# Kernel tuning notes

Hardware: AMD Instinct MI355X
Metric: run time of the kernel (lower is better)

Reference implementation:

```python
import jax, jax.numpy as jnp
import numpy as np

NUM_EXPERTS = 64
TOP_K = 2
AUX_COEF = 0.01
Z_COEF = 0.001
INIT_STD = 0.02


def setup_inputs() -> dict:
    key = jax.random.key(0)
    k1, k2 = jax.random.split(key)
    B, S, D = 4, 4096, 2048
    x = jax.random.normal(k1, (B, S, D), dtype=jnp.float32)
    gate_w = jax.random.normal(k2, (NUM_EXPERTS, D), dtype=jnp.float32) * INIT_STD
    return {"x": x, "gate_w": gate_w}


def reference(x, gate_w):
    B, S, D = x.shape
    E, K = NUM_EXPERTS, TOP_K
    # gate linear: (B,S,D) @ (D,E) -> (B,S,E), cast to fp32 like .float()
    logits = jnp.einsum('bsd,ed->bse', x, gate_w).astype(jnp.float32)
    weights = jax.nn.softmax(logits, axis=-1)
    top_weights, top_indices = jax.lax.top_k(weights, K)
    top_weights = top_weights / jnp.sum(top_weights, axis=-1, keepdims=True)
    # load-balance aux loss (training branch)
    flat_idx = top_indices.reshape(-1)
    tokens_per_expert = jax.ops.segment_sum(
        jnp.ones_like(flat_idx, dtype=jnp.float32), flat_idx, num_segments=E)
    f = tokens_per_expert / (B * S * K)
    P = jnp.mean(weights, axis=(0, 1))
    balance_loss = E * jnp.sum(f * P)
    z_loss = jnp.mean(jnp.square(jax.nn.logsumexp(logits, axis=-1)))
    aux_loss = AUX_COEF * balance_loss + Z_COEF * z_loss
    return top_indices, top_weights, aux_loss
```

## Files before the change

### kernel.cpp

```cpp
#include <hip/hip_runtime.h>
#include <math.h>

#define NTOK 16384
#define DDIM 2048
#define NEXP 64
#define NKQ 8
#define KSLICE 256
#define TPB 128

typedef __attribute__((ext_vector_type(8))) short bf16x8;
typedef __attribute__((ext_vector_type(4))) float f32x4;


__device__ __forceinline__ unsigned short f2bf(float f) {
    unsigned int u = __builtin_bit_cast(unsigned int, f);
    u += 0x7fffu + ((u >> 16) & 1u);
    return (unsigned short)(u >> 16);
}
__device__ __forceinline__ float bf2f(unsigned short s) {
    return __builtin_bit_cast(float, ((unsigned int)s) << 16);
}
__device__ __forceinline__ void split3(float x, unsigned short &h,
                                       unsigned short &m, unsigned short &l) {
    h = f2bf(x);
    float r1 = x - bf2f(h);
    m = f2bf(r1);
    float r2 = r1 - bf2f(m);
    l = f2bf(r2);
}

__global__ void k_wpack(const float* __restrict__ gw, unsigned short* __restrict__ wp) {
    int idx = blockIdx.x * 256 + threadIdx.x;
    int lane = idx & 63;
    int ks   = (idx >> 6) & 63;
    int eg   = idx >> 12;
    int e  = eg * 16 + (lane & 15);
    int k0 = ks * 32 + (lane >> 4) * 8;
    const float* src = gw + (size_t)e * DDIM + k0;
    union { unsigned short s[8]; uint4 v; } H, M, L;
    #pragma unroll
    for (int j = 0; j < 8; ++j) split3(src[j], H.s[j], M.s[j], L.s[j]);
    size_t fb = (size_t)(eg * 64 + ks) * 1536 + lane * 8;
    *(uint4*)(wp + fb)        = H.v;
    *(uint4*)(wp + fb + 512)  = M.v;
    *(uint4*)(wp + fb + 1024) = L.v;
}

__global__ __launch_bounds__(512, 4)
void k_gemm(const float* __restrict__ x, const unsigned short* __restrict__ wp,
            float* __restrict__ part) {
    __shared__ __align__(16) char Ws[49152];

    const int tid  = threadIdx.x;
    const int kq   = blockIdx.x & 7;
    const int tok0 = (blockIdx.x >> 3) * TPB;

    const int lane = tid & 63;
    const int wv   = tid >> 6;
    const int tau  = lane & 15;
    const int kap  = lane >> 4;

    const float* xb = x + (size_t)(tok0 + wv * 16 + tau) * DDIM
                        + kq * KSLICE + kap * 8;
    float4 xf[4][2];
    #pragma unroll
    for (int i = 0; i < 4; ++i) {
        xf[i][0] = *(const float4*)(xb + i * 32);
        xf[i][1] = *(const float4*)(xb + i * 32 + 4);
    }

    f32x4 acc[4];
    #pragma unroll
    for (int eg = 0; eg < 4; ++eg) acc[eg] = (f32x4){0.f, 0.f, 0.f, 0.f};

    for (int h = 0; h < 2; ++h) {
        if (h) __syncthreads();
        {
            const char* wsrc = (const char*)wp + (size_t)(kq * 8 + h * 4) * 3072;
            #pragma unroll
            for (int eg = 0; eg < 4; ++eg) {
                const char* s = wsrc + (size_t)eg * 196608;
                char* d = Ws + eg * 12288;
                #pragma unroll
                for (int r = 0; r < 2; ++r) {
                    int idx = r * 512 + tid;
                    if (idx < 768)
                        *(uint4*)(d + idx * 16) = *(const uint4*)(s + idx * 16);
                }
            }
        }
        __syncthreads();
        #pragma unroll
        for (int ks = 0; ks < 4; ++ks) {
            float4 a = xf[ks][0], b = xf[ks][1];
            union U8 { unsigned short s[8]; bf16x8 v; };
            U8 Ah, Am, Al;
            float in[8] = {a.x, a.y, a.z, a.w, b.x, b.y, b.z, b.w};
            #pragma unroll
            for (int j = 0; j < 8; ++j) split3(in[j], Ah.s[j], Am.s[j], Al.s[j]);

            if (h == 0) {
                xf[ks][0] = *(const float4*)(xb + 128 + ks * 32);
                xf[ks][1] = *(const float4*)(xb + 128 + ks * 32 + 4);
            }

            #pragma unroll
            for (int eg = 0; eg < 4; ++eg) {
                const char* wb = Ws + eg * 12288 + ks * 3072 + lane * 16;
                bf16x8 Bh = *(const bf16x8*)(wb);
                bf16x8 Bm = *(const bf16x8*)(wb + 1024);
                bf16x8 Bl = *(const bf16x8*)(wb + 2048);
                acc[eg] = __builtin_amdgcn_mfma_f32_16x16x32_bf16(Ah.v, Bh, acc[eg], 0, 0, 0);
                acc[eg] = __builtin_amdgcn_mfma_f32_16x16x32_bf16(Ah.v, Bm, acc[eg], 0, 0, 0);
                acc[eg] = __builtin_amdgcn_mfma_f32_16x16x32_bf16(Am.v, Bh, acc[eg], 0, 0, 0);
                acc[eg] = __builtin_amdgcn_mfma_f32_16x16x32_bf16(Ah.v, Bl, acc[eg], 0, 0, 0);
                acc[eg] = __builtin_amdgcn_mfma_f32_16x16x32_bf16(Al.v, Bh, acc[eg], 0, 0, 0);
                acc[eg] = __builtin_amdgcn_mfma_f32_16x16x32_bf16(Am.v, Bm, acc[eg], 0, 0, 0);
            }
        }
    }

    float* pb = part + ((size_t)kq * NTOK + tok0 + wv * 16) * 64;
    #pragma unroll
    for (int eg = 0; eg < 4; ++eg)
        #pragma unroll
        for (int j = 0; j < 4; ++j)
            pb[(kap * 4 + j) * 64 + eg * 16 + tau] = acc[eg][j];
}

__global__ __launch_bounds__(256)
void k_reduce(const float* __restrict__ part, float* __restrict__ out,
              float* __restrict__ gcnt, float* __restrict__ gP,
              float* __restrict__ gz) {
    __shared__ float Ps[NEXP], Cnt[NEXP], Zs;
    const int tid = threadIdx.x;
    if (tid < NEXP) { Ps[tid] = 0.f; Cnt[tid] = 0.f; }
    if (tid == 0) Zs = 0.f;
    __syncthreads();

    const int lane = tid & 63;
    const int wv   = tid >> 6;
    const int t0   = blockIdx.x * 16 + wv * 4;

    float v[4][8];
    #pragma unroll
    for (int i = 0; i < 4; ++i)
        #pragma unroll
        for (int q = 0; q < 8; ++q)
            v[i][q] = part[((size_t)q * NTOK + t0 + i) * 64 + lane];

    float Pacc = 0.f, zacc = 0.f;
    #pragma unroll
    for (int i = 0; i < 4; ++i) {
        float l = ((v[i][0] + v[i][1]) + (v[i][2] + v[i][3]))
                + ((v[i][4] + v[i][5]) + (v[i][6] + v[i][7]));
        float mx = l;
        #pragma unroll
        for (int off = 32; off > 0; off >>= 1) mx = fmaxf(mx, __shfl_xor(mx, off));
        float s = expf(l - mx);
        float sum = s;
        #pragma unroll
        for (int off = 32; off > 0; off >>= 1) sum += __shfl_xor(sum, off);
        Pacc += s / sum;

        unsigned long long b1 = __ballot(l == mx);
        int i1 = __ffsll(b1) - 1;
        float l2 = (lane == i1) ? -INFINITY : l;
        float m2 = l2;
        #pragma unroll
        for (int off = 32; off > 0; off >>= 1) m2 = fmaxf(m2, __shfl_xor(m2, off));
        unsigned long long b2 = __ballot(l2 == m2);
        int i2 = __ffsll(b2) - 1;

        if (lane == 0) {
            float s2  = expf(m2 - mx);
            float inv = 1.f / (1.f + s2);
            int gt = t0 + i;
            ((float2*)out)[gt]              = make_float2((float)i1, (float)i2);
            ((float2*)(out + 2 * NTOK))[gt] = make_float2(inv, s2 * inv);
            atomicAdd(&Cnt[i1], 1.f);
            atomicAdd(&Cnt[i2], 1.f);
            float lse = mx + logf(sum);
            zacc += lse * lse;
        }
    }
    atomicAdd(&Ps[lane], Pacc);
    if (lane == 0) atomicAdd(&Zs, zacc);
    __syncthreads();

    if (tid < NEXP) {
        atomicAdd(&gcnt[tid], Cnt[tid]);
        atomicAdd(&gP[tid],   Ps[tid]);
    }
    if (tid == 0) atomicAdd(gz, Zs);
}

__global__ void k_final(const float* __restrict__ ws, float* __restrict__ out) {
    int lane = threadIdx.x;
    float v = ws[lane] * ws[64 + lane];
    #pragma unroll
    for (int off = 32; off > 0; off >>= 1) v += __shfl_xor(v, off);
    if (lane == 0) {
        float bal = 64.f * v / (32768.f * 16384.f);
        float z   = ws[128] / 16384.f;
        out[4 * NTOK] = 0.01f * bal + 0.001f * z;
    }
}

extern "C" void kernel_launch(void* const* d_in, const int* in_sizes, int n_in,
                              void* d_out, int out_size, void* d_ws, size_t ws_size,
                              hipStream_t stream) {
    const float* x  = (const float*)d_in[0];
    const float* gw = (const float*)d_in[1];
    float* out = (float*)d_out;
    float* wsf = (float*)d_ws;
    unsigned short* wp = (unsigned short*)((char*)d_ws + 1024);
    float* part = (float*)((char*)d_ws + (1 << 20));

    hipMemsetAsync(d_ws, 0, 516, stream);
    k_wpack<<<64, 256, 0, stream>>>(gw, wp);
    k_gemm<<<NKQ * (NTOK / TPB), 512, 0, stream>>>(x, wp, part);
    k_reduce<<<NTOK / 16, 256, 0, stream>>>(part, out, wsf, wsf + 64, wsf + 128);
    k_final<<<1, 64, 0, stream>>>(wsf, out);
}
```

Measured before the change: 86.64 us.

## Use packed bf16 convert for splits and prefetch weight tiles via registers

Replaces the scalar software float-to-bf16 rounding in the 3-way split with the hardware v_cvt_pk_bf16_f32 instruction, which converts two floats at once. Re-lays out the packed weight buffer so that each k-quarter's tiles are contiguous. The GEMM now loads all weight tiles for both halves through registers, fetching the second half while the first half computes. This hides global load latency behind the MFMA work and cuts ALU cost in the split, at the price of 24 extra VGPRs for the weight prefetch.

```diff
diff --git a/kernel.cpp b/kernel.cpp
--- a/kernel.cpp
+++ b/kernel.cpp
@@ -12,21 +12,15 @@
 typedef __attribute__((ext_vector_type(4))) float f32x4;
 
 
-__device__ __forceinline__ unsigned short f2bf(float f) {
-    unsigned int u = __builtin_bit_cast(unsigned int, f);
-    u += 0x7fffu + ((u >> 16) & 1u);
-    return (unsigned short)(u >> 16);
-}
-__device__ __forceinline__ float bf2f(unsigned short s) {
-    return __builtin_bit_cast(float, ((unsigned int)s) << 16);
-}
-__device__ __forceinline__ void split3(float x, unsigned short &h,
-                                       unsigned short &m, unsigned short &l) {
-    h = f2bf(x);
-    float r1 = x - bf2f(h);
-    m = f2bf(r1);
-    float r2 = r1 - bf2f(m);
-    l = f2bf(r2);
+__device__ __forceinline__ void split3pk(float a, float b,
+                                         unsigned &H, unsigned &M, unsigned &L) {
+    asm("v_cvt_pk_bf16_f32 %0, %1, %2" : "=v"(H) : "v"(a), "v"(b));
+    float ra = a - __builtin_bit_cast(float, H << 16);
+    float rb = b - __builtin_bit_cast(float, H & 0xffff0000u);
+    asm("v_cvt_pk_bf16_f32 %0, %1, %2" : "=v"(M) : "v"(ra), "v"(rb));
+    float sa = ra - __builtin_bit_cast(float, M << 16);
+    float sb = rb - __builtin_bit_cast(float, M & 0xffff0000u);
+    asm("v_cvt_pk_bf16_f32 %0, %1, %2" : "=v"(L) : "v"(sa), "v"(sb));
 }
 
 __global__ void k_wpack(const float* __restrict__ gw, unsigned short* __restrict__ wp) {
@@ -37,13 +31,15 @@
     int e  = eg * 16 + (lane & 15);
     int k0 = ks * 32 + (lane >> 4) * 8;
     const float* src = gw + (size_t)e * DDIM + k0;
-    union { unsigned short s[8]; uint4 v; } H, M, L;
-    #pragma unroll
-    for (int j = 0; j < 8; ++j) split3(src[j], H.s[j], M.s[j], L.s[j]);
-    size_t fb = (size_t)(eg * 64 + ks) * 1536 + lane * 8;
-    *(uint4*)(wp + fb)        = H.v;
-    *(uint4*)(wp + fb + 512)  = M.v;
-    *(uint4*)(wp + fb + 1024) = L.v;
+    uint4 H, M, L;
+    split3pk(src[0], src[1], H.x, M.x, L.x);
+    split3pk(src[2], src[3], H.y, M.y, L.y);
+    split3pk(src[4], src[5], H.z, M.z, L.z);
+    split3pk(src[6], src[7], H.w, M.w, L.w);
+    size_t fb = ((size_t)ks * 12 + eg * 3) * 512 + lane * 8;
+    *(uint4*)(wp + fb)        = H;
+    *(uint4*)(wp + fb + 512)  = M;
+    *(uint4*)(wp + fb + 1024) = L;
 }
 
 __global__ __launch_bounds__(512, 4)
@@ -54,7 +50,6 @@
     const int tid  = threadIdx.x;
     const int kq   = blockIdx.x & 7;
     const int tok0 = (blockIdx.x >> 3) * TPB;
-
     const int lane = tid & 63;
     const int wv   = tid >> 6;
     const int tau  = lane & 15;
@@ -69,35 +64,39 @@
         xf[i][1] = *(const float4*)(xb + i * 32 + 4);
     }
 
+    const char* wsrc = (const char*)wp + (size_t)(kq * 8) * 12288;
+    uint4 wreg[6];
+    #pragma unroll
+    for (int r = 0; r < 6; ++r)
+        wreg[r] = *(const uint4*)(wsrc + (r * 512 + tid) * 16);
+
     f32x4 acc[4];
     #pragma unroll
     for (int eg = 0; eg < 4; ++eg) acc[eg] = (f32x4){0.f, 0.f, 0.f, 0.f};
 
     for (int h = 0; h < 2; ++h) {
         if (h) __syncthreads();
-        {
-            const char* wsrc = (const char*)wp + (size_t)(kq * 8 + h * 4) * 3072;
+        #pragma unroll
+        for (int r = 0; r < 6; ++r)
+            *(uint4*)(Ws + (r * 512 + tid) * 16) = wreg[r];
+        if (h == 0) {
             #pragma unroll
-            for (int eg = 0; eg < 4; ++eg) {
-                const char* s = wsrc + (size_t)eg * 196608;
-                char* d = Ws + eg * 12288;
-                #pragma unroll
-                for (int r = 0; r < 2; ++r) {
-                    int idx = r * 512 + tid;
-                    if (idx < 768)
-                        *(uint4*)(d + idx * 16) = *(const uint4*)(s + idx * 16);
-                }
-            }
+            for (int r = 0; r < 6; ++r)
+                wreg[r] = *(const uint4*)(wsrc + 49152 + (r * 512 + tid) * 16);
         }
         __syncthreads();
+
         #pragma unroll
         for (int ks = 0; ks < 4; ++ks) {
             float4 a = xf[ks][0], b = xf[ks][1];
-            union U8 { unsigned short s[8]; bf16x8 v; };
-            U8 Ah, Am, Al;
-            float in[8] = {a.x, a.y, a.z, a.w, b.x, b.y, b.z, b.w};
-            #pragma unroll
-            for (int j = 0; j < 8; ++j) split3(in[j], Ah.s[j], Am.s[j], Al.s[j]);
+            uint4 Ah, Am, Al;
+            split3pk(a.x, a.y, Ah.x, Am.x, Al.x);
+            split3pk(a.z, a.w, Ah.y, Am.y, Al.y);
+            split3pk(b.x, b.y, Ah.z, Am.z, Al.z);
+            split3pk(b.z, b.w, Ah.w, Am.w, Al.w);
+            bf16x8 Ahv = __builtin_bit_cast(bf16x8, Ah);
+            bf16x8 Amv = __builtin_bit_cast(bf16x8, Am);
+            bf16x8 Alv = __builtin_bit_cast(bf16x8, Al);
 
             if (h == 0) {
                 xf[ks][0] = *(const float4*)(xb + 128 + ks * 32);
@@ -106,16 +105,16 @@
 
             #pragma unroll
             for (int eg = 0; eg < 4; ++eg) {
-                const char* wb = Ws + eg * 12288 + ks * 3072 + lane * 16;
+                const char* wb = Ws + ks * 12288 + eg * 3072 + lane * 16;
                 bf16x8 Bh = *(const bf16x8*)(wb);
                 bf16x8 Bm = *(const bf16x8*)(wb + 1024);
                 bf16x8 Bl = *(const bf16x8*)(wb + 2048);
-                acc[eg] = __builtin_amdgcn_mfma_f32_16x16x32_bf16(Ah.v, Bh, acc[eg], 0, 0, 0);
-                acc[eg] = __builtin_amdgcn_mfma_f32_16x16x32_bf16(Ah.v, Bm, acc[eg], 0, 0, 0);
-                acc[eg] = __builtin_amdgcn_mfma_f32_16x16x32_bf16(Am.v, Bh, acc[eg], 0, 0, 0);
-                acc[eg] = __builtin_amdgcn_mfma_f32_16x16x32_bf16(Ah.v, Bl, acc[eg], 0, 0, 0);
-                acc[eg] = __builtin_amdgcn_mfma_f32_16x16x32_bf16(Al.v, Bh, acc[eg], 0, 0, 0);
-                acc[eg] = __builtin_amdgcn_mfma_f32_16x16x32_bf16(Am.v, Bm, acc[eg], 0, 0, 0);
+                acc[eg] = __builtin_amdgcn_mfma_f32_16x16x32_bf16(Ahv, Bh, acc[eg], 0, 0, 0);
+                acc[eg] = __builtin_amdgcn_mfma_f32_16x16x32_bf16(Ahv, Bm, acc[eg], 0, 0, 0);
+                acc[eg] = __builtin_amdgcn_mfma_f32_16x16x32_bf16(Amv, Bh, acc[eg], 0, 0, 0);
+                acc[eg] = __builtin_amdgcn_mfma_f32_16x16x32_bf16(Ahv, Bl, acc[eg], 0, 0, 0);
+                acc[eg] = __builtin_amdgcn_mfma_f32_16x16x32_bf16(Alv, Bh, acc[eg], 0, 0, 0);
+                acc[eg] = __builtin_amdgcn_mfma_f32_16x16x32_bf16(Amv, Bm, acc[eg], 0, 0, 0);
             }
         }
     }
```

Result: slower. 94.74 us (+9.3%).
